# Optimization experiments

Hardware: AMD Instinct MI355X
Metric: run time of the kernel (lower is better)

The kernel has to match this reference:

```python
import jax, jax.numpy as jnp
import numpy as np

B, C, CI, H, W = 8, 1024, 512, 56, 56
BN_EPS = 1e-5


def _conv1x1(x, w, b):
    # x: [B,C,H,W], w: [O,C], b: [O] -> [B,O,H,W]
    return jnp.einsum('bchw,oc->bohw', x, w) + b[None, :, None, None]


def setup_inputs() -> dict:
    key = jax.random.key(0)
    ks = jax.random.split(key, 12)
    s = lambda k, shape: (jax.random.normal(k, shape, jnp.float32) * 0.02)
    return {
        'x': jax.random.normal(ks[0], (B, C, H, W), jnp.float32),
        'theta_w': s(ks[1], (CI, C)), 'theta_b': s(ks[2], (CI,)),
        'phi_w': s(ks[3], (CI, C)), 'phi_b': s(ks[4], (CI,)),
        'g_w': s(ks[5], (CI, C)), 'g_b': s(ks[6], (CI,)),
        'wz_w': s(ks[7], (C, CI)), 'wz_b': s(ks[8], (C,)),
        'bn_gamma': 1.0 + 0.1 * jax.random.normal(ks[9], (C,), jnp.float32),
        'bn_beta': s(ks[10], (C,)),
    }


def reference(x, theta_w, theta_b, phi_w, phi_b, g_w, g_b, wz_w, wz_b, bn_gamma, bn_beta):
    b, c, h, w = x.shape
    n = h * w
    # 1x1-conv projections, flattened to token sequences
    g_x = _conv1x1(x, g_w, g_b).reshape(b, -1, n).transpose(0, 2, 1)       # [B,N,CI]
    theta_x = _conv1x1(x, theta_w, theta_b).reshape(b, -1, n).transpose(0, 2, 1)  # [B,N,CI]
    phi_x = _conv1x1(x, phi_w, phi_b).reshape(b, -1, n)                     # [B,CI,N]
    # embedded-gaussian: f = theta @ phi^T, softmax over last dim
    f = jnp.einsum('bnc,bcm->bnm', theta_x, phi_x)                          # [B,N,N]
    attn = jax.nn.softmax(f, axis=-1)
    y = jnp.einsum('bnm,bmc->bnc', attn, g_x)                               # [B,N,CI]
    y = y.transpose(0, 2, 1).reshape(b, -1, h, w)                           # [B,CI,H,W]
    z = _conv1x1(y, wz_w, wz_b)                                             # [B,C,H,W]
    # BatchNorm2d in training mode: batch statistics over (B,H,W), biased var
    mean = z.mean(axis=(0, 2, 3))
    var = z.var(axis=(0, 2, 3))
    zn = (z - mean[None, :, None, None]) * jax.lax.rsqrt(var + BN_EPS)[None, :, None, None]
    zn = zn * bn_gamma[None, :, None, None] + bn_beta[None, :, None, None]
    return zn + x
```

## Files before the change

kernel.cpp:

```cpp
#include <hip/hip_runtime.h>
#include <cstdint>
#include <cstdio>

#define DEVINL __device__ __forceinline__

typedef _Float16 f16x8 __attribute__((ext_vector_type(8)));
typedef float    f32x4 __attribute__((ext_vector_type(4)));

static constexpr int B_  = 8;
static constexpr int C_  = 1024;
static constexpr int CI_ = 512;
static constexpr int N_  = 56 * 56;
static constexpr int NP  = 3328;
static constexpr float BN_EPS = 1e-5f;

DEVINL uint16_t f2h(float f) {
  union { _Float16 h; uint16_t u; } cv;
  cv.h = (_Float16)f;
  return cv.u;
}

DEVINL void async16(const void* g, void* lds) {
  __builtin_amdgcn_global_load_lds(
      (const __attribute__((address_space(1))) uint32_t*)g,
      (__attribute__((address_space(3))) uint32_t*)lds, 16, 0, 0);
}

template <int BIAS>
__global__ __launch_bounds__(512, 2) void gemm256(
    const uint16_t* __restrict__ A, const uint16_t* __restrict__ Bt,
    uint16_t* __restrict__ Cc, const float* __restrict__ bias,
    int K, int lda, int ldb, int ldc,
    long aBatch, long bBatch, long cBatch, int nbx, int nby) {
  __shared__ uint16_t lds[65536];

  const int nwg = gridDim.x, orig = blockIdx.x;
  const int q = nwg >> 3, r = nwg & 7, xcd = orig & 7, idx = orig >> 3;
  const int wgid = (xcd < r ? xcd * (q + 1) : r * (q + 1) + (xcd - r) * q) + idx;
  const int bx = wgid % nbx;
  const int by = (wgid / nbx) % nby;
  const int zb = wgid / (nbx * nby);

  const int tid = threadIdx.x, w = tid >> 6, l = tid & 63;
  const int wm = w >> 2, wn = w & 3, lr = l & 15, lg = l >> 4;

  const uint16_t* Ab = A + (long)zb * aBatch + (long)bx * 256 * lda;
  const uint16_t* Bb = Bt + (long)zb * bBatch + (long)by * 256 * ldb;

  const int NT = K >> 6;

  const int c0 = tid, c1 = 512 + tid;
  const long aoff0 = (long)(c0 >> 2) * lda + (((c0 & 3) ^ ((c0 >> 3) & 3)) * 8);
  const long aoff1 = (long)(c1 >> 2) * lda + (((c1 & 3) ^ ((c1 >> 3) & 3)) * 8);
  const long boff0 = (long)(c0 >> 2) * ldb + (((c0 & 3) ^ ((c0 >> 3) & 3)) * 8);
  const long boff1 = (long)(c1 >> 2) * ldb + (((c1 & 3) ^ ((c1 >> 3) & 3)) * 8);
  const int ldsW0 = (w * 64) * 8;
  const int ldsW1 = (512 + w * 64) * 8;

  auto stageA = [&](int t, int ks, int buf) {
    int tw = t; while (tw >= NT) tw -= NT;
    const uint16_t* src = Ab + tw * 64 + ks * 32;
    const int reg = (buf * 2 + ks) * 8192;
    async16(src + aoff0, &lds[reg + ldsW0]);
    async16(src + aoff1, &lds[reg + ldsW1]);
  };
  auto stageB = [&](int t, int ks, int buf) {
    int tw = t; while (tw >= NT) tw -= NT;
    const uint16_t* src = Bb + tw * 64 + ks * 32;
    const int reg = 32768 + (buf * 2 + ks) * 8192;
    async16(src + boff0, &lds[reg + ldsW0]);
    async16(src + boff1, &lds[reg + ldsW1]);
  };

  const int laneSwz = (lg ^ ((lr >> 1) & 3)) * 8;
  f32x4 acc[8][4] = {};
  f16x8 af[4], bf[4];

#define LOAD_A(b, ks, mh)                                                     \
  _Pragma("unroll") for (int i = 0; i < 4; ++i) {                             \
    const int row_ = wm * 128 + ((mh) * 4 + i) * 16 + lr;                     \
    af[i] = *reinterpret_cast<const f16x8*>(                                  \
        &lds[((b) * 2 + (ks)) * 8192 + row_ * 32 + laneSwz]);                 \
  }
#define LOAD_B(b, ks)                                                         \
  _Pragma("unroll") for (int i = 0; i < 4; ++i) {                             \
    const int row_ = wn * 64 + i * 16 + lr;                                   \
    bf[i] = *reinterpret_cast<const f16x8*>(                                  \
        &lds[32768 + ((b) * 2 + (ks)) * 8192 + row_ * 32 + laneSwz]);         \
  }
#define MFMA16(mh)                                                            \
  _Pragma("unroll") for (int i = 0; i < 4; ++i)                               \
  _Pragma("unroll") for (int j = 0; j < 4; ++j)                               \
    acc[(mh) * 4 + i][j] = __builtin_amdgcn_mfma_f32_16x16x32_f16(            \
        af[i], bf[j], acc[(mh) * 4 + i][j], 0, 0, 0);
#define WAIT_LGKM()                                       \
  asm volatile("s_waitcnt lgkmcnt(0)" ::: "memory");      \
  __builtin_amdgcn_sched_barrier(0);
#define WAIT_VM8()                                        \
  asm volatile("s_waitcnt vmcnt(8)" ::: "memory");        \
  __builtin_amdgcn_sched_barrier(0);

#define TILE(t, b)                                                            \
  {                                                                           \
                                                   \
    LOAD_B(b, 0); LOAD_A(b, 0, 0);                                            \
    stageA((t) + 1, 1, (b) ^ 1);                                              \
    __builtin_amdgcn_s_barrier(); WAIT_LGKM();                                \
    __builtin_amdgcn_s_setprio(1); MFMA16(0); __builtin_amdgcn_s_setprio(0);  \
    __builtin_amdgcn_s_barrier();                                             \
                                                   \
    LOAD_A(b, 0, 1);                                                          \
    stageB((t) + 1, 1, (b) ^ 1);                                              \
    __builtin_amdgcn_s_barrier(); WAIT_LGKM();                                \
    __builtin_amdgcn_s_setprio(1); MFMA16(1); __builtin_amdgcn_s_setprio(0);  \
    WAIT_VM8();                                                               \
    __builtin_amdgcn_s_barrier();                                             \
                                                   \
    LOAD_B(b, 1); LOAD_A(b, 1, 0);                                            \
    stageA((t) + 2, 0, (b));                                                  \
    __builtin_amdgcn_s_barrier(); WAIT_LGKM();                                \
    __builtin_amdgcn_s_setprio(1); MFMA16(0); __builtin_amdgcn_s_setprio(0);  \
    __builtin_amdgcn_s_barrier();                                             \
                                                   \
    LOAD_A(b, 1, 1);                                                          \
    stageB((t) + 2, 0, (b));                                                  \
    __builtin_amdgcn_s_barrier(); WAIT_LGKM();                                \
    __builtin_amdgcn_s_setprio(1); MFMA16(1); __builtin_amdgcn_s_setprio(0);  \
    WAIT_VM8();                                                               \
    __builtin_amdgcn_s_barrier();                                             \
  }

  stageA(0, 0, 0); stageB(0, 0, 0);
  stageA(0, 1, 0); stageB(0, 1, 0);
  stageA(1, 0, 1); stageB(1, 0, 1);
  WAIT_VM8();
  __builtin_amdgcn_s_barrier();

  const int NTE = NT & ~1;
  for (int tp = 0; tp < NTE; tp += 2) {
    TILE(tp, 0);
    TILE(tp + 1, 1);
  }
  if (NT & 1) TILE(NT - 1, 0);

#undef TILE
#undef LOAD_A
#undef LOAD_B
#undef MFMA16
#undef WAIT_LGKM
#undef WAIT_VM8

  uint16_t* Cp = Cc + (long)zb * cBatch + ((long)bx * 256) * ldc + (long)by * 256;
#pragma unroll
  for (int mf = 0; mf < 8; ++mf) {
#pragma unroll
    for (int nf = 0; nf < 4; ++nf) {
      const int col = wn * 64 + nf * 16 + lr;
      const f32x4 v = acc[mf][nf];
#pragma unroll
      for (int qq = 0; qq < 4; ++qq) {
        const int row = wm * 128 + mf * 16 + lg * 4 + qq;
        float val = v[qq];
        if constexpr (BIAS == 1) val += bias[bx * 256 + row];
        if constexpr (BIAS == 2) val += bias[by * 256 + col];
        Cp[(long)row * ldc + col] = f2h(val);
      }
    }
  }
}

__global__ __launch_bounds__(256) void transpose_cast(
    const float* __restrict__ x, uint16_t* __restrict__ xT) {
  __shared__ float t[32][33];
  const int b = blockIdx.z;
  const float* xb = x + (long)b * C_ * N_;
  uint16_t* xTb = xT + (long)b * NP * C_;
  const int n0 = blockIdx.x * 32, c0 = blockIdx.y * 32;
  const int tx = threadIdx.x & 31, ty = threadIdx.x >> 5;
#pragma unroll
  for (int i = 0; i < 4; ++i) {
    const int cc = c0 + ty + i * 8, nn = n0 + tx;
    t[ty + i * 8][tx] = (nn < N_) ? xb[(long)cc * N_ + nn] : 0.f;
  }
  __syncthreads();
#pragma unroll
  for (int i = 0; i < 4; ++i) {
    const int nn = n0 + ty + i * 8, cc = c0 + tx;
    xTb[(long)nn * C_ + cc] = f2h(t[tx][ty + i * 8]);
  }
}

__global__ __launch_bounds__(256) void cvt_f16(
    const float* __restrict__ src, uint16_t* __restrict__ dst, int n) {
  int i = blockIdx.x * 256 + threadIdx.x;
  const int stride = gridDim.x * 256;
  for (; i < n; i += stride) dst[i] = f2h(src[i]);
}

__global__ __launch_bounds__(256) void concat_bias(
    const float* __restrict__ a, const float* __restrict__ b,
    float* __restrict__ d) {
  const int i = blockIdx.x * 256 + threadIdx.x;
  if (i < 512) d[i] = a[i];
  else if (i < 1024) d[i] = b[i - 512];
}

__global__ __launch_bounds__(256) void softmax_inplace(uint16_t* __restrict__ f) {
  const int row = blockIdx.x, tid = threadIdx.x;
  uint16_t* p = f + ((long)blockIdx.y * NP + row) * NP;
  __shared__ float buf[N_];
  __shared__ float red[8];
  float mx = -3.4e38f;
  for (int ch = tid; ch < N_ / 8; ch += 256) {
    const f16x8 v = *reinterpret_cast<const f16x8*>(p + ch * 8);
#pragma unroll
    for (int j = 0; j < 8; ++j) {
      const float fv = (float)v[j];
      buf[ch * 8 + j] = fv;
      mx = fmaxf(mx, fv);
    }
  }
  for (int o = 32; o; o >>= 1) mx = fmaxf(mx, __shfl_xor(mx, o));
  if ((tid & 63) == 0) red[tid >> 6] = mx;
  __syncthreads();
  mx = fmaxf(fmaxf(red[0], red[1]), fmaxf(red[2], red[3]));

  float s = 0.f;
  for (int i = tid; i < N_; i += 256) {
    const float e = __expf(buf[i] - mx);
    buf[i] = e;
    s += e;
  }
  for (int o = 32; o; o >>= 1) s += __shfl_xor(s, o);
  __syncthreads();
  if ((tid & 63) == 0) red[tid >> 6] = s;
  __syncthreads();
  const float rinv = 1.0f / (red[0] + red[1] + red[2] + red[3]);

  for (int ch = tid; ch < N_ / 8; ch += 256) {
    f16x8 o8;
#pragma unroll
    for (int j = 0; j < 8; ++j) o8[j] = (_Float16)(buf[ch * 8 + j] * rinv);
    *reinterpret_cast<f16x8*>(p + ch * 8) = o8;
  }
}

__global__ __launch_bounds__(256) void bn_stats(
    const _Float16* __restrict__ z, const float* __restrict__ gamma,
    const float* __restrict__ beta, float* __restrict__ ss) {
  const int c = blockIdx.x, tid = threadIdx.x;
  float sum = 0.f, sq = 0.f;
  for (int b = 0; b < B_; ++b) {
    const _Float16* zp = z + ((long)b * C_ + c) * NP;
    for (int ch = tid; ch < N_ / 8; ch += 256) {
      const f16x8 v = *(const f16x8*)(zp + ch * 8);
#pragma unroll
      for (int j = 0; j < 8; ++j) {
        const float fv = (float)v[j];
        sum += fv;
        sq += fv * fv;
      }
    }
  }
  for (int o = 32; o; o >>= 1) {
    sum += __shfl_xor(sum, o);
    sq += __shfl_xor(sq, o);
  }
  __shared__ float r1[8], r2[8];
  if ((tid & 63) == 0) { r1[tid >> 6] = sum; r2[tid >> 6] = sq; }
  __syncthreads();
  if (tid == 0) {
    sum = r1[0] + r1[1] + r1[2] + r1[3];
    sq  = r2[0] + r2[1] + r2[2] + r2[3];
    const float inv_n = 1.0f / (float)(B_ * N_);
    const float mean = sum * inv_n;
    const float var = sq * inv_n - mean * mean;
    const float sc = gamma[c] * rsqrtf(var + BN_EPS);
    ss[c] = sc;
    ss[C_ + c] = beta[c] - mean * sc;
  }
}

__global__ __launch_bounds__(256) void bn_apply(
    const _Float16* __restrict__ z, const float* __restrict__ x,
    const float* __restrict__ ss, float* __restrict__ out) {
  constexpr int CH = N_ / 8;
  const long nv = (long)B_ * C_ * CH;
  const long stride = (long)gridDim.x * 256;
  for (long v = (long)blockIdx.x * 256 + threadIdx.x; v < nv; v += stride) {
    const long row = v / CH;
    const int ch = (int)(v % CH);
    const int c = (int)(row % C_);
    const f16x8 zz = *(const f16x8*)(z + row * NP + ch * 8);
    const float4 x0 = *(const float4*)(x + row * (long)N_ + ch * 8);
    const float4 x1 = *(const float4*)(x + row * (long)N_ + ch * 8 + 4);
    const float sc = ss[c], sh = ss[C_ + c];
    float4 o0, o1;
    o0.x = (float)zz[0] * sc + sh + x0.x;
    o0.y = (float)zz[1] * sc + sh + x0.y;
    o0.z = (float)zz[2] * sc + sh + x0.z;
    o0.w = (float)zz[3] * sc + sh + x0.w;
    o1.x = (float)zz[4] * sc + sh + x1.x;
    o1.y = (float)zz[5] * sc + sh + x1.y;
    o1.z = (float)zz[6] * sc + sh + x1.z;
    o1.w = (float)zz[7] * sc + sh + x1.w;
    *(float4*)(out + row * (long)N_ + ch * 8) = o0;
    *(float4*)(out + row * (long)N_ + ch * 8 + 4) = o1;
  }
}

extern "C" void kernel_launch(void* const* d_in, const int* in_sizes, int n_in,
                              void* d_out, int out_size, void* d_ws,
                              size_t ws_size, hipStream_t stream) {
  const float* x       = (const float*)d_in[0];
  const float* theta_w = (const float*)d_in[1];
  const float* theta_b = (const float*)d_in[2];
  const float* phi_w   = (const float*)d_in[3];
  const float* phi_b   = (const float*)d_in[4];
  const float* g_w     = (const float*)d_in[5];
  const float* g_b     = (const float*)d_in[6];
  const float* wz_w    = (const float*)d_in[7];
  const float* wz_b    = (const float*)d_in[8];
  const float* gamma   = (const float*)d_in[9];
  const float* beta    = (const float*)d_in[10];
  float* out = (float*)d_out;

  char* ws = (char*)d_ws;
  size_t off = 0;
  auto alloc = [&](size_t bytes) {
    void* p = ws + off;
    off += (bytes + 255) & ~(size_t)255;
    return p;
  };
  uint16_t* wfused = (uint16_t*)alloc((size_t)1024 * 1024 * 2);
  uint16_t* wg     = (uint16_t*)alloc((size_t)CI_ * C_ * 2);
  uint16_t* wzh    = (uint16_t*)alloc((size_t)C_ * CI_ * 2);
  float*    bfused = (float*)alloc((size_t)1024 * 4);
  uint16_t* projT  = (uint16_t*)alloc((size_t)B_ * NP * 1024 * 2);
  uint16_t* gbuf   = (uint16_t*)alloc((size_t)B_ * CI_ * NP * 2);
  uint16_t* ybuf   = (uint16_t*)alloc((size_t)B_ * NP * CI_ * 2);
  uint16_t* zbuf   = (uint16_t*)alloc((size_t)B_ * C_ * NP * 2);
  float*    ss     = (float*)alloc((size_t)C_ * 2 * 4);

  const size_t xTb = (size_t)B_ * NP * C_ * 2;
  const size_t fB  = (size_t)B_ * NP * NP * 2;
  uint16_t* xT    = (uint16_t*)alloc(fB > xTb ? fB : xTb);
  uint16_t* fattn = xT;
  if (off > ws_size) {
    fprintf(stderr, "kernel_launch: workspace too small: need %zu have %zu\n",
            off, ws_size);
    return;
  }

  cvt_f16<<<512, 256, 0, stream>>>(theta_w, wfused, CI_ * C_);
  cvt_f16<<<512, 256, 0, stream>>>(phi_w, wfused + 512 * 1024, CI_ * C_);
  cvt_f16<<<512, 256, 0, stream>>>(g_w, wg, CI_ * C_);
  cvt_f16<<<512, 256, 0, stream>>>(wz_w, wzh, C_ * CI_);
  concat_bias<<<4, 256, 0, stream>>>(theta_b, phi_b, bfused);

  transpose_cast<<<dim3(NP / 32, C_ / 32, B_), 256, 0, stream>>>(x, xT);

  gemm256<2><<<dim3(B_ * NP / 256 * 4), 512, 0, stream>>>(
      xT, wfused, projT, bfused, C_, C_, C_, 1024,
      0, 0, 0, B_ * NP / 256, 4);
  gemm256<1><<<dim3(2 * 13 * B_), 512, 0, stream>>>(
      wg, xT, gbuf, g_b, C_, C_, C_, NP,
      0, (long)NP * C_, (long)CI_ * NP, 2, 13);

  gemm256<0><<<dim3(13 * 13 * B_), 512, 0, stream>>>(
      projT, projT + 512, fattn, nullptr, CI_, 1024, 1024, NP,
      (long)NP * 1024, (long)NP * 1024, (long)NP * NP, 13, 13);
  softmax_inplace<<<dim3(N_, B_), 256, 0, stream>>>(fattn);

  gemm256<0><<<dim3(13 * 2 * B_), 512, 0, stream>>>(
      fattn, gbuf, ybuf, nullptr, N_, NP, NP, CI_,
      (long)NP * NP, (long)CI_ * NP, (long)NP * CI_, 13, 2);

  gemm256<1><<<dim3(4 * 13 * B_), 512, 0, stream>>>(
      wzh, ybuf, zbuf, wz_b, CI_, CI_, CI_, NP,
      0, (long)NP * CI_, (long)C_ * NP, 4, 13);

  bn_stats<<<C_, 256, 0, stream>>>((const _Float16*)zbuf, gamma, beta, ss);
  bn_apply<<<4096, 256, 0, stream>>>((const _Float16*)zbuf, x, ss, out);
}
```

Measured before the change: 514.3 us.

## Use nontemporal stores, column-major GEMM tile order, and merge weight casts

Output stores in the GEMM epilogue, transpose, softmax and bn_apply become nontemporal, so streamed results bypass the caches. A colMajor flag changes how workgroups map to tiles for two GEMMs, grouping tiles that share the same A rows for better L2 reuse. The four weight-cast launches are merged into one kernel to cut launch overhead. The risks are that nontemporal stores may hurt when the next kernel reads the data back soon (softmax output feeds the next GEMM), and that the tile-order change may reduce reuse of the other operand.

```diff
diff --git a/kernel.cpp b/kernel.cpp
--- a/kernel.cpp
+++ b/kernel.cpp
@@ -31,14 +31,15 @@
     const uint16_t* __restrict__ A, const uint16_t* __restrict__ Bt,
     uint16_t* __restrict__ Cc, const float* __restrict__ bias,
     int K, int lda, int ldb, int ldc,
-    long aBatch, long bBatch, long cBatch, int nbx, int nby) {
+    long aBatch, long bBatch, long cBatch, int nbx, int nby, int colMajor) {
   __shared__ uint16_t lds[65536];
 
   const int nwg = gridDim.x, orig = blockIdx.x;
   const int q = nwg >> 3, r = nwg & 7, xcd = orig & 7, idx = orig >> 3;
   const int wgid = (xcd < r ? xcd * (q + 1) : r * (q + 1) + (xcd - r) * q) + idx;
-  const int bx = wgid % nbx;
-  const int by = (wgid / nbx) % nby;
+  const int rest = wgid % (nbx * nby);
+  const int bx = colMajor ? rest / nby : rest % nbx;
+  const int by = colMajor ? rest % nby : rest / nbx;
   const int zb = wgid / (nbx * nby);
 
   const int tid = threadIdx.x, w = tid >> 6, l = tid & 63;
@@ -163,7 +164,7 @@
         float val = v[qq];
         if constexpr (BIAS == 1) val += bias[bx * 256 + row];
         if constexpr (BIAS == 2) val += bias[by * 256 + col];
-        Cp[(long)row * ldc + col] = f2h(val);
+        __builtin_nontemporal_store(f2h(val), &Cp[(long)row * ldc + col]);
       }
     }
   }
@@ -186,15 +187,27 @@
 #pragma unroll
   for (int i = 0; i < 4; ++i) {
     const int nn = n0 + ty + i * 8, cc = c0 + tx;
-    xTb[(long)nn * C_ + cc] = f2h(t[tx][ty + i * 8]);
-  }
-}
-
-__global__ __launch_bounds__(256) void cvt_f16(
-    const float* __restrict__ src, uint16_t* __restrict__ dst, int n) {
-  int i = blockIdx.x * 256 + threadIdx.x;
+    __builtin_nontemporal_store(f2h(t[tx][ty + i * 8]), &xTb[(long)nn * C_ + cc]);
+  }
+}
+
+__global__ __launch_bounds__(256) void cvt_f16_all(
+    const float* __restrict__ s0, uint16_t* __restrict__ d0, int n0,
+    const float* __restrict__ s1, uint16_t* __restrict__ d1, int n1,
+    const float* __restrict__ s2, uint16_t* __restrict__ d2, int n2,
+    const float* __restrict__ s3, uint16_t* __restrict__ d3, int n3) {
   const int stride = gridDim.x * 256;
-  for (; i < n; i += stride) dst[i] = f2h(src[i]);
+  const int total = n0 + n1 + n2 + n3;
+  for (int i = blockIdx.x * 256 + threadIdx.x; i < total; i += stride) {
+    int j = i;
+    if (j < n0) { d0[j] = f2h(s0[j]); continue; }
+    j -= n0;
+    if (j < n1) { d1[j] = f2h(s1[j]); continue; }
+    j -= n1;
+    if (j < n2) { d2[j] = f2h(s2[j]); continue; }
+    j -= n2;
+    d3[j] = f2h(s3[j]);
+  }
 }
 
 __global__ __launch_bounds__(256) void concat_bias(
@@ -241,7 +254,7 @@
     f16x8 o8;
 #pragma unroll
     for (int j = 0; j < 8; ++j) o8[j] = (_Float16)(buf[ch * 8 + j] * rinv);
-    *reinterpret_cast<f16x8*>(p + ch * 8) = o8;
+    __builtin_nontemporal_store(o8, reinterpret_cast<f16x8*>(p + ch * 8));
   }
 }
 
@@ -292,20 +305,16 @@
     const int ch = (int)(v % CH);
     const int c = (int)(row % C_);
     const f16x8 zz = *(const f16x8*)(z + row * NP + ch * 8);
-    const float4 x0 = *(const float4*)(x + row * (long)N_ + ch * 8);
-    const float4 x1 = *(const float4*)(x + row * (long)N_ + ch * 8 + 4);
+    const f32x4 x0 = *(const f32x4*)(x + row * (long)N_ + ch * 8);
+    const f32x4 x1 = *(const f32x4*)(x + row * (long)N_ + ch * 8 + 4);
     const float sc = ss[c], sh = ss[C_ + c];
-    float4 o0, o1;
-    o0.x = (float)zz[0] * sc + sh + x0.x;
-    o0.y = (float)zz[1] * sc + sh + x0.y;
-    o0.z = (float)zz[2] * sc + sh + x0.z;
-    o0.w = (float)zz[3] * sc + sh + x0.w;
-    o1.x = (float)zz[4] * sc + sh + x1.x;
-    o1.y = (float)zz[5] * sc + sh + x1.y;
-    o1.z = (float)zz[6] * sc + sh + x1.z;
-    o1.w = (float)zz[7] * sc + sh + x1.w;
-    *(float4*)(out + row * (long)N_ + ch * 8) = o0;
-    *(float4*)(out + row * (long)N_ + ch * 8 + 4) = o1;
+    f32x4 o0, o1;
+#pragma unroll
+    for (int j = 0; j < 4; ++j) o0[j] = (float)zz[j] * sc + sh + x0[j];
+#pragma unroll
+    for (int j = 0; j < 4; ++j) o1[j] = (float)zz[4 + j] * sc + sh + x1[j];
+    __builtin_nontemporal_store(o0, (f32x4*)(out + row * (long)N_ + ch * 8));
+    __builtin_nontemporal_store(o1, (f32x4*)(out + row * (long)N_ + ch * 8 + 4));
   }
 }
 
@@ -352,33 +361,34 @@
     return;
   }
 
-  cvt_f16<<<512, 256, 0, stream>>>(theta_w, wfused, CI_ * C_);
-  cvt_f16<<<512, 256, 0, stream>>>(phi_w, wfused + 512 * 1024, CI_ * C_);
-  cvt_f16<<<512, 256, 0, stream>>>(g_w, wg, CI_ * C_);
-  cvt_f16<<<512, 256, 0, stream>>>(wz_w, wzh, C_ * CI_);
+  cvt_f16_all<<<512, 256, 0, stream>>>(
+      theta_w, wfused, CI_ * C_,
+      phi_w, wfused + 512 * 1024, CI_ * C_,
+      g_w, wg, CI_ * C_,
+      wz_w, wzh, C_ * CI_);
   concat_bias<<<4, 256, 0, stream>>>(theta_b, phi_b, bfused);
 
   transpose_cast<<<dim3(NP / 32, C_ / 32, B_), 256, 0, stream>>>(x, xT);
 
   gemm256<2><<<dim3(B_ * NP / 256 * 4), 512, 0, stream>>>(
       xT, wfused, projT, bfused, C_, C_, C_, 1024,
-      0, 0, 0, B_ * NP / 256, 4);
+      0, 0, 0, B_ * NP / 256, 4, 1);
   gemm256<1><<<dim3(2 * 13 * B_), 512, 0, stream>>>(
       wg, xT, gbuf, g_b, C_, C_, C_, NP,
-      0, (long)NP * C_, (long)CI_ * NP, 2, 13);
+      0, (long)NP * C_, (long)CI_ * NP, 2, 13, 0);
 
   gemm256<0><<<dim3(13 * 13 * B_), 512, 0, stream>>>(
       projT, projT + 512, fattn, nullptr, CI_, 1024, 1024, NP,
-      (long)NP * 1024, (long)NP * 1024, (long)NP * NP, 13, 13);
+      (long)NP * 1024, (long)NP * 1024, (long)NP * NP, 13, 13, 0);
   softmax_inplace<<<dim3(N_, B_), 256, 0, stream>>>(fattn);
 
   gemm256<0><<<dim3(13 * 2 * B_), 512, 0, stream>>>(
       fattn, gbuf, ybuf, nullptr, N_, NP, NP, CI_,
-      (long)NP * NP, (long)CI_ * NP, (long)NP * CI_, 13, 2);
+      (long)NP * NP, (long)CI_ * NP, (long)NP * CI_, 13, 2, 1);
 
   gemm256<1><<<dim3(4 * 13 * B_), 512, 0, stream>>>(
       wzh, ybuf, zbuf, wz_b, CI_, CI_, CI_, NP,
-      0, (long)NP * CI_, (long)C_ * NP, 4, 13);
+      0, (long)NP * CI_, (long)C_ * NP, 4, 13, 0);
 
   bn_stats<<<C_, 256, 0, stream>>>((const _Float16*)zbuf, gamma, beta, ss);
   bn_apply<<<4096, 256, 0, stream>>>((const _Float16*)zbuf, x, ss, out);
```

New measurement: 592.9 us. 1.15x slower.
